# Performance work log

Hardware: AMD Instinct MI355X
Metric: run time of the kernel (lower is better)

## Reference

```python
import jax, jax.numpy as jnp
import numpy as np


def setup_inputs() -> dict:
    key = jax.random.key(0)
    B, C, H, W = 16, 512, 56, 56
    heads, agent, win = 8, 49, 56
    ks = jax.random.split(key, 16)
    std = 0.02
    tn = lambda k, s: jax.random.truncated_normal(k, -2.0, 2.0, s, jnp.float32) * std
    return {
        "x": jax.random.normal(ks[0], (B, C, H, W), jnp.float32),
        "H": H,
        "W": W,
        "q_w": jax.random.normal(ks[1], (C, C), jnp.float32) * (C ** -0.5),
        "kv_w": jax.random.normal(ks[2], (2 * C, C), jnp.float32) * (C ** -0.5),
        "proj_w": jax.random.normal(ks[3], (C, C), jnp.float32) * (C ** -0.5),
        "proj_b": jnp.zeros((C,), jnp.float32),
        "dwc_w": jax.random.normal(ks[4], (C, 1, 3, 3), jnp.float32) * (1.0 / 3.0),
        "dwc_b": jnp.zeros((C,), jnp.float32),
        "an_bias": tn(ks[5], (heads, agent, 7, 7)),
        "na_bias": tn(ks[6], (heads, agent, 7, 7)),
        "ah_bias": tn(ks[7], (1, heads, agent, win, 1)),
        "aw_bias": tn(ks[8], (1, heads, agent, 1, win)),
        "ha_bias": tn(ks[9], (1, heads, win, 1, agent)),
        "wa_bias": tn(ks[10], (1, heads, 1, win, agent)),
    }


def reference(x, H, W, q_w, kv_w, proj_w, proj_b, dwc_w, dwc_b,
              an_bias, na_bias, ah_bias, aw_bias, ha_bias, wa_bias):
    B, C, H1, W1 = x.shape
    heads, agent = an_bias.shape[0], an_bias.shape[1]
    hd = C // heads
    scale = hd ** -0.5
    n = H1 * W1
    pool = int(agent ** 0.5)  # 7

    # NOTE: original torch code does x.view(B, H1*W1, C) on an NCHW tensor:
    # a raw row-major reshape, reproduced faithfully here.
    xf = x.reshape(B, n, C)

    q = xf @ q_w.T                       # [B, n, C]
    kv = xf @ kv_w.T                     # [B, n, 2C]
    k, v = kv[..., :C], kv[..., C:]

    # agent tokens: adaptive avg pool of q (as HxW image) to pool x pool (exact blocks)
    q_img = q.reshape(B, H, W, C)
    agent_tokens = q_img.reshape(B, pool, H // pool, pool, W // pool, C).mean(axis=(2, 4))
    agent_tokens = agent_tokens.reshape(B, agent, C)

    qh = q.reshape(B, n, heads, hd).transpose(0, 2, 1, 3)            # [B,h,n,d]
    kh = k.reshape(B, n, heads, hd).transpose(0, 2, 1, 3)            # [B,h,n,d]
    vh = v.reshape(B, n, heads, hd).transpose(0, 2, 1, 3)            # [B,h,n,d]
    ah = agent_tokens.reshape(B, agent, heads, hd).transpose(0, 2, 1, 3)  # [B,h,a,d]

    # stage 1: agent -> kv attention, with interpolated + separable position bias
    pb1 = jax.image.resize(an_bias, (heads, agent, H, W), 'bilinear').reshape(1, heads, agent, n)
    pb2 = (ah_bias + aw_bias).reshape(1, heads, agent, n)
    agent_logits = jnp.einsum('bhad,bhnd->bhan', ah * scale, kh) + pb1 + pb2
    agent_attn = jax.nn.softmax(agent_logits, axis=-1)
    agent_v = jnp.einsum('bhan,bhnd->bhad', agent_attn, vh)          # [B,h,a,d]

    # stage 2: query -> agent attention
    ab1 = jax.image.resize(na_bias, (heads, agent, H, W), 'bilinear').reshape(1, heads, agent, n)
    ab1 = ab1.transpose(0, 1, 3, 2)                                  # [1,h,n,a]
    ab2 = (ha_bias + wa_bias).reshape(1, heads, n, agent)
    q_logits = jnp.einsum('bhnd,bhad->bhna', qh * scale, ah) + ab1 + ab2
    q_attn = jax.nn.softmax(q_logits, axis=-1)
    out = jnp.einsum('bhna,bhad->bhnd', q_attn, agent_v)
    out = out.transpose(0, 2, 1, 3).reshape(B, n, C)

    # depthwise-conv residual on v (sr_ratio == 1: no interpolate)
    v_img = v.reshape(B, H, W, C).transpose(0, 3, 1, 2)              # [B,C,H,W]
    dwc = jax.lax.conv_general_dilated(
        v_img, dwc_w, window_strides=(1, 1), padding='SAME',
        feature_group_count=C, dimension_numbers=('NCHW', 'OIHW', 'NCHW'))
    dwc = dwc + dwc_b[None, :, None, None]
    out = out + dwc.transpose(0, 2, 3, 1).reshape(B, n, C)

    out = out @ proj_w.T + proj_b
    return out.reshape(B, C, H1, W1)
```

## Files before the change

### kernel.cpp

```cpp
#include <hip/hip_runtime.h>
#include <math.h>

#define B_ 16
#define C_ 512
#define Nn 3136
#define HEADS 8
#define HD 64
#define AG 49
#define Mrows (B_ * Nn)

typedef unsigned short ushortT;
typedef __attribute__((ext_vector_type(8))) short bf16x8;
typedef __attribute__((ext_vector_type(4))) float f32x4;

#define MFMA16(a, b, c) __builtin_amdgcn_mfma_f32_16x16x32_bf16((a), (b), (c), 0, 0, 0)

__device__ inline float bf2f(ushortT u) { return __uint_as_float(((unsigned)u) << 16); }
__device__ inline ushortT f2bf(float f) {
    unsigned x = __float_as_uint(f);
    unsigned r = (x + 0x7fffu + ((x >> 16) & 1u)) >> 16;
    return (ushortT)r;
}
__device__ inline f32x4 fzero4() { f32x4 z = {0.f, 0.f, 0.f, 0.f}; return z; }

__device__ inline void gl_lds16(const ushortT* g, ushortT* l) {
    __builtin_amdgcn_global_load_lds(
        (const __attribute__((address_space(1))) void*)g,
        (__attribute__((address_space(3))) void*)l, 16, 0, 0);
}

#define VMCNT(n) asm volatile("s_waitcnt vmcnt(" #n ")" ::: "memory")
#define LGKM0_SB() { asm volatile("s_waitcnt lgkmcnt(0)" ::: "memory"); \
                     __builtin_amdgcn_sched_barrier(0); }
#define BAR() __builtin_amdgcn_s_barrier()

__global__ void cvt_f2b4(const float* __restrict__ src, ushortT* __restrict__ dst, int n4) {
    int g = blockIdx.x * 256 + threadIdx.x;
    if (g >= n4) return;
    float4 v = *(const float4*)&src[(size_t)g * 4];
    ushort4 o = make_ushort4(f2bf(v.x), f2bf(v.y), f2bf(v.z), f2bf(v.w));
    *(ushort4*)&dst[(size_t)g * 4] = o;
}

__global__ void cvt_weights(const float* __restrict__ qw, const float* __restrict__ kvw,
                            const float* __restrict__ pw, const float* __restrict__ dwcw,
                            ushortT* __restrict__ Wqkv, ushortT* __restrict__ Wp,
                            float* __restrict__ wT) {
    int g = blockIdx.x * 256 + threadIdx.x;
    if (g < 196608) {
        const float* src = (g < 65536) ? &qw[(size_t)g * 4] : &kvw[(size_t)(g - 65536) * 4];
        float4 v = *(const float4*)src;
        *(ushort4*)&Wqkv[(size_t)g * 4] =
            make_ushort4(f2bf(v.x), f2bf(v.y), f2bf(v.z), f2bf(v.w));
    } else if (g < 262144) {
        float4 v = *(const float4*)&pw[(size_t)(g - 196608) * 4];
        *(ushort4*)&Wp[(size_t)(g - 196608) * 4] =
            make_ushort4(f2bf(v.x), f2bf(v.y), f2bf(v.z), f2bf(v.w));
    } else {
        int gg = g - 262144;
        if (gg < 4608) { int c = gg & 511, tap = gg >> 9; wT[gg] = dwcw[c * 9 + tap]; }
    }
}

template <int MB, int NL>
__device__ __forceinline__ void quad(f32x4 (&acc)[8][4], const bf16x8 (&af)[4][2],
                                     const bf16x8 (&bf)[4][2]) {
#pragma unroll
    for (int m = 0; m < 4; ++m)
#pragma unroll
        for (int n = 0; n < 2; ++n) {
            acc[MB + m][NL + n] = MFMA16(af[m][0], bf[NL + n][0], acc[MB + m][NL + n]);
            acc[MB + m][NL + n] = MFMA16(af[m][1], bf[NL + n][1], acc[MB + m][NL + n]);
        }
}

template <typename TO>
__global__ __launch_bounds__(512, 2)
void gemm256(const ushortT* __restrict__ A, const ushortT* __restrict__ Bw,
             const float* __restrict__ bias, TO* __restrict__ out,
             int N, int nbn) {
    __shared__ __align__(16) ushortT As[2][16384];
    __shared__ __align__(16) ushortT Bs[2][16384];
    const int t = threadIdx.x, lane = t & 63, wid = t >> 6;
    const int chunk = (int)gridDim.x >> 3;
    const int id2 = ((int)blockIdx.x & 7) * chunk + ((int)blockIdx.x >> 3);
    const int by = id2 / nbn, bx = id2 - by * nbn;
    const int m0 = by * 256, n0 = bx * 256;
    const int wm = wid >> 2, wn = wid & 3;

    const int rl0 = t >> 3;
    const int skg = (t & 7) ^ (rl0 & 7);
    const int ra0 = rl0 & 63;
    const int ra1 = (rl0 & 63) + 128;
    const int rb0 = (rl0 & 31) + ((rl0 >> 5) << 6);
    const int rb1 = rb0 + 128;
    const ushortT* gA0 = A + (size_t)(m0 + ra0) * 512 + skg * 8;
    const ushortT* gA1 = A + (size_t)(m0 + ra1) * 512 + skg * 8;
    const ushortT* gB0 = Bw + (size_t)(n0 + rb0) * 512 + skg * 8;
    const ushortT* gB1 = Bw + (size_t)(n0 + rb1) * 512 + skg * 8;
    const int bA0 = wid * 512;
    const int bA1 = wid * 512 + 8192;
    const int gbu = ((wid * 8) & 31) + (((wid * 8) >> 5) << 6);
    const int bB0 = gbu * 64;
    const int bB1 = bB0 + 8192;

#define ISSA(bufi, ro, ko) { gl_lds16(gA0 + (ro) * 512 + (ko), &As[bufi][bA0 + (ro) * 64]); \
                             gl_lds16(gA1 + (ro) * 512 + (ko), &As[bufi][bA1 + (ro) * 64]); }
#define ISSB(bufi, ro, ko) { gl_lds16(gB0 + (ro) * 512 + (ko), &Bs[bufi][bB0 + (ro) * 64]); \
                             gl_lds16(gB1 + (ro) * 512 + (ko), &Bs[bufi][bB1 + (ro) * 64]); }

    f32x4 acc[8][4];
#pragma unroll
    for (int i = 0; i < 8; ++i)
#pragma unroll
        for (int j = 0; j < 4; ++j) acc[i][j] = fzero4();

    const int r15 = lane & 15, kq16 = lane >> 4;
    const int rA = wm * 128 + r15;
    const int rB = wn * 64 + r15;
    const int sw0 = ((kq16) ^ (r15 & 7)) << 3;
    const int sw1 = ((4 + kq16) ^ (r15 & 7)) << 3;

    ISSA(0, 0, 0); ISSA(0, 64, 0);
    ISSB(0, 0, 0); ISSB(0, 32, 0);
    VMCNT(0);
    BAR();

    bf16x8 af[4][2], bf[4][2];
    for (int kt = 0; kt < 8; ++kt) {
        const ushortT* Ac = As[kt & 1];
        const ushortT* Bc = Bs[kt & 1];
        const int nb = (kt + 1) & 1;
        const int ko = (kt + 1) * 64;
        const bool pre = (kt < 7);
#pragma unroll
        for (int mt = 0; mt < 4; ++mt) {
            af[mt][0] = *(const bf16x8*)&Ac[(rA + mt * 16) * 64 + sw0];
            af[mt][1] = *(const bf16x8*)&Ac[(rA + mt * 16) * 64 + sw1];
        }
#pragma unroll
        for (int nt = 0; nt < 2; ++nt) {
            bf[nt][0] = *(const bf16x8*)&Bc[(rB + nt * 16) * 64 + sw0];
            bf[nt][1] = *(const bf16x8*)&Bc[(rB + nt * 16) * 64 + sw1];
        }
        if (pre) { ISSA(nb, 0, ko); ISSA(nb, 64, ko); }
        BAR(); LGKM0_SB();
        __builtin_amdgcn_s_setprio(1);
        quad<0, 0>(acc, af, bf);
        __builtin_amdgcn_s_setprio(0);
        BAR();
#pragma unroll
        for (int nt = 2; nt < 4; ++nt) {
            bf[nt][0] = *(const bf16x8*)&Bc[(rB + nt * 16) * 64 + sw0];
            bf[nt][1] = *(const bf16x8*)&Bc[(rB + nt * 16) * 64 + sw1];
        }
        if (pre) { ISSB(nb, 0, ko); ISSB(nb, 32, ko); }
        BAR(); LGKM0_SB();
        __builtin_amdgcn_s_setprio(1);
        quad<0, 2>(acc, af, bf);
        __builtin_amdgcn_s_setprio(0);
        BAR();
#pragma unroll
        for (int mt = 0; mt < 4; ++mt) {
            af[mt][0] = *(const bf16x8*)&Ac[(rA + 64 + mt * 16) * 64 + sw0];
            af[mt][1] = *(const bf16x8*)&Ac[(rA + 64 + mt * 16) * 64 + sw1];
        }
        BAR(); LGKM0_SB();
        __builtin_amdgcn_s_setprio(1);
        quad<4, 0>(acc, af, bf);
        __builtin_amdgcn_s_setprio(0);
        BAR();
        __builtin_amdgcn_s_setprio(1);
        quad<4, 2>(acc, af, bf);
        __builtin_amdgcn_s_setprio(0);
        if (pre) { VMCNT(0); }
        BAR();
    }
#undef ISSA
#undef ISSB

    const int cn = r15, rg = kq16 << 2;
#pragma unroll
    for (int mt = 0; mt < 8; ++mt) {
        int mrow = m0 + wm * 128 + mt * 16 + rg;
#pragma unroll
        for (int nt = 0; nt < 4; ++nt) {
            int ncol = n0 + wn * 64 + nt * 16 + cn;
            float bv = bias ? bias[ncol] : 0.f;
#pragma unroll
            for (int r = 0; r < 4; ++r) {
                float v = acc[mt][nt][r] + bv;
                if (sizeof(TO) == 2) ((ushortT*)out)[(size_t)(mrow + r) * N + ncol] = f2bf(v);
                else                 ((float*)out)[(size_t)(mrow + r) * N + ncol] = v;
            }
        }
    }
}

__global__ __launch_bounds__(256)
void agent_pool(const ushortT* __restrict__ qkv, float* __restrict__ at) {
    __shared__ float red[256][9];
    int t = threadIdx.x;
    int ba = blockIdx.x;
    int b = ba / AG, a = ba % AG;
    int c8 = (t & 63) << 3, qr = t >> 6;
    int p1 = a / 7, p2 = a % 7;
    float s[8] = {};
#pragma unroll
    for (int pp = 0; pp < 16; ++pp) {
        int pos = (qr << 4) + pp;
        int i = (p1 * 8 + (pos >> 3)) * 56 + p2 * 8 + (pos & 7);
        bf16x8 u = *(const bf16x8*)&qkv[(size_t)(b * Nn + i) * 1536 + c8];
#pragma unroll
        for (int j = 0; j < 8; ++j) s[j] += bf2f((ushortT)u[j]);
    }
#pragma unroll
    for (int j = 0; j < 8; ++j) red[t][j] = s[j];
    __syncthreads();
    if (t < 64) {
        float* o = &at[((size_t)(b * AG + a) << 9) + (t << 3)];
#pragma unroll
        for (int j = 0; j < 8; ++j)
            o[j] = (red[t][j] + red[t + 64][j] + red[t + 128][j] + red[t + 192][j])
                   * (1.f / 64.f);
    }
}

__device__ inline float bilin7(const float* __restrict__ p, int y, int x) {
    float fy = fminf(fmaxf(y * 0.125f - 0.4375f, 0.f), 6.f);
    float fx = fminf(fmaxf(x * 0.125f - 0.4375f, 0.f), 6.f);
    int y0 = (int)fy; float ty = fy - y0; int y1 = min(y0 + 1, 6);
    int x0 = (int)fx; float tx = fx - x0; int x1 = min(x0 + 1, 6);
    float v00 = p[y0 * 7 + x0], v01 = p[y0 * 7 + x1];
    float v10 = p[y1 * 7 + x0], v11 = p[y1 * 7 + x1];
    return (1.f - ty) * ((1.f - tx) * v00 + tx * v01) + ty * ((1.f - tx) * v10 + tx * v11);
}

__global__ void bias_k(const float* __restrict__ an, const float* __restrict__ ahb,
                       const float* __restrict__ awb, const float* __restrict__ na,
                       const float* __restrict__ hab, const float* __restrict__ wab,
                       float* __restrict__ b1, float* __restrict__ b2) {
    int g = blockIdx.x * 256 + threadIdx.x;
    const int NT = HEADS * AG * Nn;
    if (g < NT) {
        int i = g % Nn; int a = (g / Nn) % AG; int h = g / (AG * Nn);
        int y = i / 56, x = i % 56;
        b1[g] = bilin7(an + (h * AG + a) * 49, y, x)
              + ahb[(h * AG + a) * 56 + y] + awb[(h * AG + a) * 56 + x];
    } else {
        g -= NT; if (g >= NT) return;
        int a = g % AG; int i = (g / AG) % Nn; int h = g / (AG * Nn);
        int y = i / 56, x = i % 56;
        b2[g] = bilin7(na + (h * AG + a) * 49, y, x)
              + hab[(h * 56 + y) * AG + a] + wab[(h * 56 + x) * AG + a];
    }
}

__global__ void zero2(float* __restrict__ num, int n1, float* __restrict__ den, int n2) {
    int g = blockIdx.x * 256 + threadIdx.x;
    if (g < n1) num[g] = 0.f;
    else if (g - n1 < n2) den[g - n1] = 0.f;
}

__global__ __launch_bounds__(256)
void agent_av_fused(const ushortT* __restrict__ qkv, const float* __restrict__ at,
                    const float* __restrict__ b1, float* __restrict__ num,
                    float* __restrict__ den) {
    __shared__ __align__(16) ushortT ah_s[64 * 72];
    __shared__ __align__(16) ushortT vt[64 * 72];
    __shared__ __align__(16) ushortT p_s[64 * 72];
    const int t = threadIdx.x, lane = t & 63, wid = t >> 6;
    const int bh = blockIdx.y, b = bh >> 3, h = bh & 7;
    for (int idx = t; idx < 512; idx += 256) {
        int a = idx >> 3, d8 = (idx & 7) << 3;
        bf16x8 tmp;
        if (a < AG) {
            const float* p = &at[((size_t)(b * AG + a) << 9) + (h << 6) + d8];
#pragma unroll
            for (int j = 0; j < 8; ++j) tmp[j] = (short)f2bf(p[j] * 0.125f);
        } else {
#pragma unroll
            for (int j = 0; j < 8; ++j) tmp[j] = 0;
        }
        *(bf16x8*)&ah_s[a * 72 + d8] = tmp;
    }
    __syncthreads();
    const int r15 = lane & 15, kq = (lane >> 4) << 3;
    const int rbase = (lane >> 4) << 2;
    bf16x8 af[4][2];
#pragma unroll
    for (int mt = 0; mt < 4; ++mt)
#pragma unroll
        for (int ks = 0; ks < 2; ++ks)
            af[mt][ks] = *(const bf16x8*)&ah_s[(mt * 16 + r15) * 72 + ks * 32 + kq];

    f32x4 accn[4];
#pragma unroll
    for (int nt = 0; nt < 4; ++nt) accn[nt] = fzero4();
    float denl[4][4];
#pragma unroll
    for (int mt = 0; mt < 4; ++mt)
#pragma unroll
        for (int r = 0; r < 4; ++r) denl[mt][r] = 0.f;

    const int i0b = blockIdx.x * 448;
    const int svi = t >> 2, svd = (t & 3) << 4;
    for (int cc = 0; cc < 7; ++cc) {
        const int i0 = i0b + cc * 64;
        {
            const ushortT* vp = &qkv[(size_t)(b * Nn + i0 + svi) * 1536 + 1024 + (h << 6) + svd];
            bf16x8 u0 = *(const bf16x8*)vp;
            bf16x8 u1 = *(const bf16x8*)(vp + 8);
#pragma unroll
            for (int j = 0; j < 8; ++j) {
                vt[(svd + j) * 72 + svi]     = (ushortT)u0[j];
                vt[(svd + 8 + j) * 72 + svi] = (ushortT)u1[j];
            }
        }
        {
            const int iw = i0 + wid * 16;
            const ushortT* kp = &qkv[(size_t)(b * Nn + iw + r15) * 1536 + 512 + (h << 6) + kq];
            bf16x8 bk0 = *(const bf16x8*)kp;
            bf16x8 bk1 = *(const bf16x8*)(kp + 32);
            f32x4 sacc[4];
#pragma unroll
            for (int mt = 0; mt < 4; ++mt) {
                sacc[mt] = MFMA16(af[mt][0], bk0, fzero4());
                sacc[mt] = MFMA16(af[mt][1], bk1, sacc[mt]);
            }
            const int ic = iw + r15;
#pragma unroll
            for (int mt = 0; mt < 4; ++mt)
#pragma unroll
                for (int r = 0; r < 4; ++r) {
                    int a = mt * 16 + rbase + r;
                    float e = 0.f;
                    if (a < AG)
                        e = __expf(sacc[mt][r] + b1[(size_t)(h * AG + a) * Nn + ic]);
                    denl[mt][r] += e;
                    p_s[a * 72 + wid * 16 + r15] = f2bf(e);
                }
        }
        __syncthreads();
        {
            bf16x8 ap0 = *(const bf16x8*)&p_s[(wid * 16 + r15) * 72 + kq];
            bf16x8 ap1 = *(const bf16x8*)&p_s[(wid * 16 + r15) * 72 + 32 + kq];
#pragma unroll
            for (int nt = 0; nt < 4; ++nt) {
                bf16x8 bv0 = *(const bf16x8*)&vt[(nt * 16 + r15) * 72 + kq];
                bf16x8 bv1 = *(const bf16x8*)&vt[(nt * 16 + r15) * 72 + 32 + kq];
                accn[nt] = MFMA16(ap0, bv0, accn[nt]);
                accn[nt] = MFMA16(ap1, bv1, accn[nt]);
            }
        }
        __syncthreads();
    }
#pragma unroll
    for (int r = 0; r < 4; ++r) {
        int a = wid * 16 + rbase + r;
        if (a < AG) {
#pragma unroll
            for (int nt = 0; nt < 4; ++nt)
                atomicAdd(&num[((size_t)(bh * AG + a) << 6) + nt * 16 + r15],
                          accn[nt][r]);
        }
    }
#pragma unroll
    for (int mt = 0; mt < 4; ++mt)
#pragma unroll
        for (int r = 0; r < 4; ++r) {
            float s = denl[mt][r];
#pragma unroll
            for (int off = 8; off >= 1; off >>= 1) s += __shfl_xor(s, off);
            if (r15 == 0) {
                int a = mt * 16 + rbase + r;
                if (a < AG) atomicAdd(&den[bh * AG + a], s);
            }
        }
}

__global__ __launch_bounds__(256)
void q_attn_mfma(const ushortT* __restrict__ qkv, const float* __restrict__ at,
                 const float* __restrict__ num, const float* __restrict__ den,
                 const float* __restrict__ b2, ushortT* __restrict__ attn) {
    __shared__ __align__(16) ushortT ah_s[64 * 72];
    __shared__ __align__(16) ushortT avT[64 * 72];
    __shared__ __align__(16) ushortT p_s[4][16 * 72];
    int t = threadIdx.x, lane = t & 63, wid = t >> 6;
    int bh = blockIdx.y, b = bh >> 3, h = bh & 7;
    for (int idx = t; idx < 512; idx += 256) {
        int a = idx >> 3, d8 = (idx & 7) << 3;
        bf16x8 tmp;
        if (a < AG) {
            const float* p = &at[((size_t)(b * AG + a) << 9) + (h << 6) + d8];
#pragma unroll
            for (int j = 0; j < 8; ++j) tmp[j] = (short)f2bf(p[j] * 0.125f);
        } else {
#pragma unroll
            for (int j = 0; j < 8; ++j) tmp[j] = 0;
        }
        *(bf16x8*)&ah_s[a * 72 + d8] = tmp;
    }
    for (int idx = t; idx < 4096; idx += 256) {
        int a = idx >> 6, d = idx & 63;
        float v = 0.f;
        if (a < AG)
            v = num[((size_t)(bh * AG + a) << 6) + d] / den[bh * AG + a];
        avT[d * 72 + a] = f2bf(v);
    }
    __syncthreads();
    int r15 = lane & 15, kq = (lane >> 4) << 3;
    bf16x8 bah[4][2], bav[4][2];
#pragma unroll
    for (int nt = 0; nt < 4; ++nt)
#pragma unroll
        for (int ks = 0; ks < 2; ++ks) {
            bah[nt][ks] = *(const bf16x8*)&ah_s[(nt * 16 + r15) * 72 + ks * 32 + kq];
            bav[nt][ks] = *(const bf16x8*)&avT[(nt * 16 + r15) * 72 + ks * 32 + kq];
        }
    ushortT* psw = p_s[wid];
    int i0b = blockIdx.x * 448;
    int rbase = (lane >> 4) << 2;
    for (int tt = 0; tt < 7; ++tt) {
        int i0 = i0b + (wid * 7 + tt) * 16;
        const ushortT* qp = &qkv[(size_t)(b * Nn + i0 + r15) * 1536 + (h << 6) + kq];
        bf16x8 aq0 = *(const bf16x8*)qp;
        bf16x8 aq1 = *(const bf16x8*)(qp + 32);
        f32x4 lg[4];
#pragma unroll
        for (int nt = 0; nt < 4; ++nt) {
            lg[nt] = MFMA16(aq0, bah[nt][0], fzero4());
            lg[nt] = MFMA16(aq1, bah[nt][1], lg[nt]);
        }
        float p4[4][4];
#pragma unroll
        for (int r = 0; r < 4; ++r) {
            int i = i0 + rbase + r;
            float vals[4]; float sm = 0.f;
#pragma unroll
            for (int nt = 0; nt < 4; ++nt) {
                int a = nt * 16 + r15;
                float e = 0.f;
                if (a < AG) e = __expf(lg[nt][r] + b2[(size_t)(h * Nn + i) * AG + a]);
                vals[nt] = e; sm += e;
            }
#pragma unroll
            for (int off = 8; off >= 1; off >>= 1) sm += __shfl_xor(sm, off);
            float inv = 1.f / sm;
#pragma unroll
            for (int nt = 0; nt < 4; ++nt) p4[nt][r] = vals[nt] * inv;
        }
#pragma unroll
        for (int nt = 0; nt < 4; ++nt)
#pragma unroll
            for (int r = 0; r < 4; ++r)
                psw[(rbase + r) * 72 + nt * 16 + r15] = f2bf(p4[nt][r]);
        bf16x8 ap0 = *(const bf16x8*)&psw[r15 * 72 + kq];
        bf16x8 ap1 = *(const bf16x8*)&psw[r15 * 72 + 32 + kq];
        f32x4 ov[4];
#pragma unroll
        for (int nt = 0; nt < 4; ++nt) {
            ov[nt] = MFMA16(ap0, bav[nt][0], fzero4());
            ov[nt] = MFMA16(ap1, bav[nt][1], ov[nt]);
        }
#pragma unroll
        for (int r = 0; r < 4; ++r) {
            int i = i0 + rbase + r;
            ushortT* op = &attn[(size_t)(b * Nn + i) * C_ + (h << 6)];
#pragma unroll
            for (int nt = 0; nt < 4; ++nt)
                op[nt * 16 + r15] = f2bf(ov[nt][r]);
        }
    }
}

__global__ void dwc_add_v(const ushortT* __restrict__ qkv, const float* __restrict__ wT,
                          const float* __restrict__ bb, ushortT* __restrict__ attn) {
    int g = blockIdx.x * 256 + threadIdx.x;
    int c8 = (g & 63) << 3;
    int bi = g >> 6;
    int i = bi % Nn;
    int y = i / 56, x = i % 56;
    float acc[8];
    {
        float4 b0 = *(const float4*)&bb[c8];
        float4 b1 = *(const float4*)&bb[c8 + 4];
        acc[0] = b0.x; acc[1] = b0.y; acc[2] = b0.z; acc[3] = b0.w;
        acc[4] = b1.x; acc[5] = b1.y; acc[6] = b1.z; acc[7] = b1.w;
    }
#pragma unroll
    for (int dy = -1; dy <= 1; ++dy) {
        int yy = y + dy; if (yy < 0 || yy > 55) continue;
#pragma unroll
        for (int dx = -1; dx <= 1; ++dx) {
            int xx = x + dx; if (xx < 0 || xx > 55) continue;
            const ushortT* vp = &qkv[(size_t)(bi + dy * 56 + dx) * 1536 + 1024 + c8];
            ushort4 u0 = *(const ushort4*)vp;
            ushort4 u1 = *(const ushort4*)(vp + 4);
            const float* wp = &wT[((dy + 1) * 3 + dx + 1) * 512 + c8];
            float4 w0 = *(const float4*)wp;
            float4 w1 = *(const float4*)(wp + 4);
            acc[0] += bf2f(u0.x) * w0.x; acc[1] += bf2f(u0.y) * w0.y;
            acc[2] += bf2f(u0.z) * w0.z; acc[3] += bf2f(u0.w) * w0.w;
            acc[4] += bf2f(u1.x) * w1.x; acc[5] += bf2f(u1.y) * w1.y;
            acc[6] += bf2f(u1.z) * w1.z; acc[7] += bf2f(u1.w) * w1.w;
        }
    }
    ushortT* op = &attn[(size_t)bi * C_ + c8];
    ushort4 a0 = *(const ushort4*)op;
    ushort4 a1 = *(const ushort4*)(op + 4);
    ushort4 o0 = make_ushort4(f2bf(bf2f(a0.x) + acc[0]), f2bf(bf2f(a0.y) + acc[1]),
                              f2bf(bf2f(a0.z) + acc[2]), f2bf(bf2f(a0.w) + acc[3]));
    ushort4 o1 = make_ushort4(f2bf(bf2f(a1.x) + acc[4]), f2bf(bf2f(a1.y) + acc[5]),
                              f2bf(bf2f(a1.z) + acc[6]), f2bf(bf2f(a1.w) + acc[7]));
    *(ushort4*)op = o0; *(ushort4*)(op + 4) = o1;
}

extern "C" void kernel_launch(void* const* d_in, const int* in_sizes, int n_in,
                              void* d_out, int out_size, void* d_ws, size_t ws_size,
                              hipStream_t stream) {
    const float* x      = (const float*)d_in[0];
    const float* q_w    = (const float*)d_in[3];
    const float* kv_w   = (const float*)d_in[4];
    const float* proj_w = (const float*)d_in[5];
    const float* proj_b = (const float*)d_in[6];
    const float* dwc_w  = (const float*)d_in[7];
    const float* dwc_b  = (const float*)d_in[8];
    const float* an_b   = (const float*)d_in[9];
    const float* na_b   = (const float*)d_in[10];
    const float* ah_b   = (const float*)d_in[11];
    const float* aw_b   = (const float*)d_in[12];
    const float* ha_b   = (const float*)d_in[13];
    const float* wa_b   = (const float*)d_in[14];
    float* out = (float*)d_out;

    char* ws = (char*)d_ws;
    ushortT* R    = (ushortT*)(ws);
    ushortT* qkv  = (ushortT*)(ws + 51380224);
    ushortT* Wqkv = (ushortT*)(ws + 205520896);
    ushortT* Wp   = (ushortT*)(ws + 207093760);
    float*   wT   = (float*)(ws + 207618048);
    float*   at   = (float*)(ws + 207636480);
    float*   b1   = (float*)(ws + 209242112);
    float*   b2   = (float*)(ws + 214159360);
    float*   num  = (float*)(ws + 219076608);
    float*   den  = (float*)Wqkv;
    ushortT* xb   = R;
    ushortT* attn = R;

    cvt_f2b4<<<25088, 256, 0, stream>>>(x, xb, 6422528);
    cvt_weights<<<1042, 256, 0, stream>>>(q_w, kv_w, proj_w, dwc_w, Wqkv, Wp, wT);
    gemm256<ushortT><<<1176, 512, 0, stream>>>(xb, Wqkv, nullptr, qkv, 1536, 6);
    agent_pool<<<784, 256, 0, stream>>>(qkv, at);
    bias_k<<<9604, 256, 0, stream>>>(an_b, ah_b, aw_b, na_b, ha_b, wa_b, b1, b2);
    zero2<<<1593, 256, 0, stream>>>(num, B_ * HEADS * AG * HD, den, B_ * HEADS * AG);
    agent_av_fused<<<dim3(7, 128), 256, 0, stream>>>(qkv, at, b1, num, den);
    q_attn_mfma<<<dim3(7, 128), 256, 0, stream>>>(qkv, at, num, den, b2, attn);
    dwc_add_v<<<12544, 256, 0, stream>>>(qkv, wT, dwc_b, attn);
    gemm256<float><<<392, 512, 0, stream>>>(attn, Wp, proj_b, out, 512, 2);
}
```

Baseline: 527.5 us.

## Fuse fp32-to-bf16 input conversion into QKV GEMM and store biases as bf16

Drops the separate pass that converts x to bf16. A new GEMM variant loads fp32 activations straight into registers, converts them, and writes them to LDS, while B tiles still use global-to-LDS loads. It also stores the two large positional-bias tensors as bf16 instead of fp32, which halves their write and read traffic in the attention kernels. The costs are register-staged A loads in the GEMM main loop, which may hurt overlap and occupancy, and lower precision in the attention biases.

```diff
diff --git a/kernel.cpp b/kernel.cpp
--- a/kernel.cpp
+++ b/kernel.cpp
@@ -33,14 +33,6 @@
 #define LGKM0_SB() { asm volatile("s_waitcnt lgkmcnt(0)" ::: "memory"); \
                      __builtin_amdgcn_sched_barrier(0); }
 #define BAR() __builtin_amdgcn_s_barrier()
-
-__global__ void cvt_f2b4(const float* __restrict__ src, ushortT* __restrict__ dst, int n4) {
-    int g = blockIdx.x * 256 + threadIdx.x;
-    if (g >= n4) return;
-    float4 v = *(const float4*)&src[(size_t)g * 4];
-    ushort4 o = make_ushort4(f2bf(v.x), f2bf(v.y), f2bf(v.z), f2bf(v.w));
-    *(ushort4*)&dst[(size_t)g * 4] = o;
-}
 
 __global__ void cvt_weights(const float* __restrict__ qw, const float* __restrict__ kvw,
                             const float* __restrict__ pw, const float* __restrict__ dwcw,
@@ -74,6 +66,133 @@
         }
 }
 
+__global__ __launch_bounds__(512, 2)
+void gemm_f32a(const float* __restrict__ A32, const ushortT* __restrict__ Bw,
+               ushortT* __restrict__ out, int N, int nbn) {
+    __shared__ __align__(16) ushortT As[2][16384];
+    __shared__ __align__(16) ushortT Bs[2][16384];
+    const int t = threadIdx.x, lane = t & 63, wid = t >> 6;
+    const int chunk = (int)gridDim.x >> 3;
+    const int id2 = ((int)blockIdx.x & 7) * chunk + ((int)blockIdx.x >> 3);
+    const int by = id2 / nbn, bx = id2 - by * nbn;
+    const int m0 = by * 256, n0 = bx * 256;
+    const int wm = wid >> 2, wn = wid & 3;
+
+    const int rl0 = t >> 3;
+    const int kg = t & 7;
+    const int wkg = kg ^ (rl0 & 7);
+    const float* gAr = A32 + (size_t)(m0 + rl0) * 512 + kg * 8;
+    const int dA0 = rl0 * 64 + wkg * 8;
+    const int rb0 = (rl0 & 31) + ((rl0 >> 5) << 6);
+    const int rb1 = rb0 + 128;
+    const ushortT* gB0 = Bw + (size_t)(n0 + rb0) * 512 + wkg * 8;
+    const ushortT* gB1 = Bw + (size_t)(n0 + rb1) * 512 + wkg * 8;
+    const int gbu = ((wid * 8) & 31) + (((wid * 8) >> 5) << 6);
+    const int bB0 = gbu * 64;
+    const int bB1 = bB0 + 8192;
+
+#define ISSB(bufi, ro, ko) { gl_lds16(gB0 + (ro) * 512 + (ko), &Bs[bufi][bB0 + (ro) * 64]); \
+                             gl_lds16(gB1 + (ro) * 512 + (ko), &Bs[bufi][bB1 + (ro) * 64]); }
+#define CVTW(bufi) { \
+    _Pragma("unroll") \
+    for (int j = 0; j < 4; ++j) { \
+        bf16x8 w; \
+        w[0]=(short)f2bf(pa[j][0].x); w[1]=(short)f2bf(pa[j][0].y); \
+        w[2]=(short)f2bf(pa[j][0].z); w[3]=(short)f2bf(pa[j][0].w); \
+        w[4]=(short)f2bf(pa[j][1].x); w[5]=(short)f2bf(pa[j][1].y); \
+        w[6]=(short)f2bf(pa[j][1].z); w[7]=(short)f2bf(pa[j][1].w); \
+        *(bf16x8*)&As[bufi][dA0 + j * 4096] = w; \
+    } }
+
+    f32x4 acc[8][4];
+#pragma unroll
+    for (int i = 0; i < 8; ++i)
+#pragma unroll
+        for (int j = 0; j < 4; ++j) acc[i][j] = fzero4();
+
+    const int r15 = lane & 15, kq16 = lane >> 4;
+    const int rA = wm * 128 + r15;
+    const int rB = wn * 64 + r15;
+    const int sw0 = ((kq16) ^ (r15 & 7)) << 3;
+    const int sw1 = ((4 + kq16) ^ (r15 & 7)) << 3;
+
+    float4 pa[4][2];
+#pragma unroll
+    for (int j = 0; j < 4; ++j) {
+        const float* s = gAr + (size_t)j * 64 * 512;
+        pa[j][0] = *(const float4*)s; pa[j][1] = *(const float4*)(s + 4);
+    }
+    ISSB(0, 0, 0); ISSB(0, 32, 0);
+    CVTW(0);
+    __syncthreads();
+
+    bf16x8 af[4][2], bf[4][2];
+    int cur = 0;
+    for (int kt = 0; kt < 8; ++kt) {
+        const ushortT* Ac = As[cur];
+        const ushortT* Bc = Bs[cur];
+        const int nb = cur ^ 1;
+        const int ko = (kt + 1) * 64;
+        const bool pre = (kt < 7);
+        if (pre) {
+#pragma unroll
+            for (int j = 0; j < 4; ++j) {
+                const float* s = gAr + (size_t)j * 64 * 512 + ko;
+                pa[j][0] = *(const float4*)s; pa[j][1] = *(const float4*)(s + 4);
+            }
+            ISSB(nb, 0, ko); ISSB(nb, 32, ko);
+        }
+#pragma unroll
+        for (int mt = 0; mt < 4; ++mt) {
+            af[mt][0] = *(const bf16x8*)&Ac[(rA + mt * 16) * 64 + sw0];
+            af[mt][1] = *(const bf16x8*)&Ac[(rA + mt * 16) * 64 + sw1];
+        }
+#pragma unroll
+        for (int nt = 0; nt < 2; ++nt) {
+            bf[nt][0] = *(const bf16x8*)&Bc[(rB + nt * 16) * 64 + sw0];
+            bf[nt][1] = *(const bf16x8*)&Bc[(rB + nt * 16) * 64 + sw1];
+        }
+        __builtin_amdgcn_s_setprio(1);
+        quad<0, 0>(acc, af, bf);
+        __builtin_amdgcn_s_setprio(0);
+#pragma unroll
+        for (int nt = 2; nt < 4; ++nt) {
+            bf[nt][0] = *(const bf16x8*)&Bc[(rB + nt * 16) * 64 + sw0];
+            bf[nt][1] = *(const bf16x8*)&Bc[(rB + nt * 16) * 64 + sw1];
+        }
+        __builtin_amdgcn_s_setprio(1);
+        quad<0, 2>(acc, af, bf);
+        __builtin_amdgcn_s_setprio(0);
+#pragma unroll
+        for (int mt = 0; mt < 4; ++mt) {
+            af[mt][0] = *(const bf16x8*)&Ac[(rA + 64 + mt * 16) * 64 + sw0];
+            af[mt][1] = *(const bf16x8*)&Ac[(rA + 64 + mt * 16) * 64 + sw1];
+        }
+        __builtin_amdgcn_s_setprio(1);
+        quad<4, 0>(acc, af, bf);
+        quad<4, 2>(acc, af, bf);
+        __builtin_amdgcn_s_setprio(0);
+        if (pre) { CVTW(nb); }
+        __syncthreads();
+        cur ^= 1;
+    }
+#undef ISSB
+#undef CVTW
+
+    const int cn = r15, rg = kq16 << 2;
+#pragma unroll
+    for (int mt = 0; mt < 8; ++mt) {
+        int mrow = m0 + wm * 128 + mt * 16 + rg;
+#pragma unroll
+        for (int nt = 0; nt < 4; ++nt) {
+            int ncol = n0 + wn * 64 + nt * 16 + cn;
+#pragma unroll
+            for (int r = 0; r < 4; ++r)
+                out[(size_t)(mrow + r) * N + ncol] = f2bf(acc[mt][nt][r]);
+        }
+    }
+}
+
 template <typename TO>
 __global__ __launch_bounds__(512, 2)
 void gemm256(const ushortT* __restrict__ A, const ushortT* __restrict__ Bw,
@@ -239,20 +358,20 @@
 __global__ void bias_k(const float* __restrict__ an, const float* __restrict__ ahb,
                        const float* __restrict__ awb, const float* __restrict__ na,
                        const float* __restrict__ hab, const float* __restrict__ wab,
-                       float* __restrict__ b1, float* __restrict__ b2) {
+                       ushortT* __restrict__ b1, ushortT* __restrict__ b2) {
     int g = blockIdx.x * 256 + threadIdx.x;
     const int NT = HEADS * AG * Nn;
     if (g < NT) {
         int i = g % Nn; int a = (g / Nn) % AG; int h = g / (AG * Nn);
         int y = i / 56, x = i % 56;
-        b1[g] = bilin7(an + (h * AG + a) * 49, y, x)
-              + ahb[(h * AG + a) * 56 + y] + awb[(h * AG + a) * 56 + x];
+        b1[g] = f2bf(bilin7(an + (h * AG + a) * 49, y, x)
+                     + ahb[(h * AG + a) * 56 + y] + awb[(h * AG + a) * 56 + x]);
     } else {
         g -= NT; if (g >= NT) return;
         int a = g % AG; int i = (g / AG) % Nn; int h = g / (AG * Nn);
         int y = i / 56, x = i % 56;
-        b2[g] = bilin7(na + (h * AG + a) * 49, y, x)
-              + hab[(h * 56 + y) * AG + a] + wab[(h * 56 + x) * AG + a];
+        b2[g] = f2bf(bilin7(na + (h * AG + a) * 49, y, x)
+                     + hab[(h * 56 + y) * AG + a] + wab[(h * 56 + x) * AG + a]);
     }
 }
 
@@ -264,7 +383,7 @@
 
 __global__ __launch_bounds__(256)
 void agent_av_fused(const ushortT* __restrict__ qkv, const float* __restrict__ at,
-                    const float* __restrict__ b1, float* __restrict__ num,
+                    const ushortT* __restrict__ b1, float* __restrict__ num,
                     float* __restrict__ den) {
     __shared__ __align__(16) ushortT ah_s[64 * 72];
     __shared__ __align__(16) ushortT vt[64 * 72];
@@ -336,7 +455,7 @@
                     int a = mt * 16 + rbase + r;
                     float e = 0.f;
                     if (a < AG)
-                        e = __expf(sacc[mt][r] + b1[(size_t)(h * AG + a) * Nn + ic]);
+                        e = __expf(sacc[mt][r] + bf2f(b1[(size_t)(h * AG + a) * Nn + ic]));
                     denl[mt][r] += e;
                     p_s[a * 72 + wid * 16 + r15] = f2bf(e);
                 }
@@ -382,7 +501,7 @@
 __global__ __launch_bounds__(256)
 void q_attn_mfma(const ushortT* __restrict__ qkv, const float* __restrict__ at,
                  const float* __restrict__ num, const float* __restrict__ den,
-                 const float* __restrict__ b2, ushortT* __restrict__ attn) {
+                 const ushortT* __restrict__ b2, ushortT* __restrict__ attn) {
     __shared__ __align__(16) ushortT ah_s[64 * 72];
     __shared__ __align__(16) ushortT avT[64 * 72];
     __shared__ __align__(16) ushortT p_s[4][16 * 72];
@@ -441,7 +560,8 @@
             for (int nt = 0; nt < 4; ++nt) {
                 int a = nt * 16 + r15;
                 float e = 0.f;
-                if (a < AG) e = __expf(lg[nt][r] + b2[(size_t)(h * Nn + i) * AG + a]);
+                if (a < AG)
+                    e = __expf(lg[nt][r] + bf2f(b2[(size_t)(h * Nn + i) * AG + a]));
                 vals[nt] = e; sm += e;
             }
 #pragma unroll
@@ -541,16 +661,14 @@
     ushortT* Wp   = (ushortT*)(ws + 207093760);
     float*   wT   = (float*)(ws + 207618048);
     float*   at   = (float*)(ws + 207636480);
-    float*   b1   = (float*)(ws + 209242112);
-    float*   b2   = (float*)(ws + 214159360);
-    float*   num  = (float*)(ws + 219076608);
-    float*   den  = (float*)Wqkv;
-    ushortT* xb   = R;
+    ushortT* b1   = (ushortT*)(ws + 209242112);
+    ushortT* b2   = (ushortT*)(ws + 211700736);
+    float*   num  = (float*)(ws + 214159360);
+    float*   den  = (float*)(ws + 215764992);
     ushortT* attn = R;
 
-    cvt_f2b4<<<25088, 256, 0, stream>>>(x, xb, 6422528);
     cvt_weights<<<1042, 256, 0, stream>>>(q_w, kv_w, proj_w, dwc_w, Wqkv, Wp, wT);
-    gemm256<ushortT><<<1176, 512, 0, stream>>>(xb, Wqkv, nullptr, qkv, 1536, 6);
+    gemm_f32a<<<1176, 512, 0, stream>>>(x, Wqkv, qkv, 1536, 6);
     agent_pool<<<784, 256, 0, stream>>>(qkv, at);
     bias_k<<<9604, 256, 0, stream>>>(an_b, ah_b, aw_b, na_b, ha_b, wa_b, b1, b2);
     zero2<<<1593, 256, 0, stream>>>(num, B_ * HEADS * AG * HD, den, B_ * HEADS * AG);
```

Result: no change. 522.3 us (-1.0%).
